# Kernel tuning notes

Hardware: AMD Instinct MI355X
Metric: run time of the kernel (lower is better)

Reference implementation:

```python
import jax, jax.numpy as jnp
import numpy as np
import math

B_SZ, T, D_IN, D_OUT, N = 8, 4096, 128, 128, 256
MAX_PHASE, RMIN, RMAX = math.pi, 0.0, 1.0


def setup_inputs() -> dict:
    key = jax.random.key(0)
    ks = jax.random.split(key, 9)
    x = jax.random.normal(ks[0], (B_SZ, T, D_IN), dtype=jnp.float32)
    # lambda parameterization exactly as in LRU.__init__
    u1 = jax.random.uniform(ks[1], (N,), minval=1e-4, maxval=1.0)
    u2 = jax.random.uniform(ks[2], (N,), minval=1e-4, maxval=1.0)
    nu_log = jnp.log(-0.5 * jnp.log(u1 * (RMAX + RMIN) * (RMAX - RMIN) + RMIN ** 2))
    theta_log = jnp.log(MAX_PHASE * u2)
    lam_abs = jnp.exp(-jnp.exp(nu_log))
    gamma_log = jnp.log(jnp.sqrt(1.0 - jnp.square(lam_abs)))
    B_re = jax.random.normal(ks[3], (N, D_IN)) / math.sqrt(2 * D_IN)
    B_im = jax.random.normal(ks[4], (N, D_IN)) / math.sqrt(2 * D_IN)
    C_re = jax.random.normal(ks[5], (D_OUT, N)) / math.sqrt(N)
    C_im = jax.random.normal(ks[6], (D_OUT, N)) / math.sqrt(N)
    D = jax.random.normal(ks[7], (D_OUT, D_IN)) / math.sqrt(D_IN)
    return {"x": x, "nu_log": nu_log, "theta_log": theta_log, "gamma_log": gamma_log,
            "B_re": B_re, "B_im": B_im, "C_re": C_re, "C_im": C_im, "D": D}


def _binary_op_diag(e1, e2):
    a1, b1 = e1
    a2, b2 = e2
    return a1 * a2, a2 * b1 + b2


def reference(x, nu_log, theta_log, gamma_log, B_re, B_im, C_re, C_im, D):
    # ss_params()
    lam_abs = jnp.exp(-jnp.exp(nu_log))
    phase = jnp.exp(theta_log)
    lam = (lam_abs * jnp.cos(phase) + 1j * (lam_abs * jnp.sin(phase))).astype(jnp.complex64)  # [N]
    gammas = jnp.exp(gamma_log)[:, None]
    Bc = (gammas * (B_re + 1j * B_im)).astype(jnp.complex64)  # [N, D_IN]
    Cc = (C_re + 1j * C_im).astype(jnp.complex64)             # [D_OUT, N]
    # diagonal complex linear recurrence via associative scan over time
    Bu = x.astype(Bc.dtype) @ Bc.T                            # [B, T, N] complex
    lam_el = jnp.broadcast_to(lam, Bu.shape)                  # [B, T, N]
    _, states = jax.lax.associative_scan(_binary_op_diag, (lam_el, Bu), axis=1)
    y = jnp.real(states @ Cc.T) + x @ D.T                     # [B, T, D_OUT]
    return y
```

## Files before the change

### kernel.cpp

```cpp
#include <hip/hip_runtime.h>
#include <math.h>

#define B_SZ 8
#define T_LEN 4096
#define D_IN 128
#define D_OUT 128
#define N_ST 256
#define BT (B_SZ * T_LEN)
#define CHUNK 64
#define NCHUNK (T_LEN / CHUNK)
#define NBLK (B_SZ * NCHUNK)

typedef __attribute__((ext_vector_type(8))) short short8;
typedef __attribute__((ext_vector_type(4))) float f32x4;
typedef unsigned int uint;
typedef unsigned short ushort;

static __device__ __forceinline__ short f2bf(float f) {
  union { float f; uint u; } v; v.f = f;
  uint r = v.u + 0x7FFFu + ((v.u >> 16) & 1u);
  return (short)(r >> 16);
}
static __device__ __forceinline__ float bf2f(uint h) {
  union { uint u; float f; } v; v.u = h << 16;
  return v.f;
}
static __device__ __forceinline__ uint pack2(float a, float b) {
  return (uint)(ushort)f2bf(a) | ((uint)(ushort)f2bf(b) << 16);
}

__global__ __launch_bounds__(256) void k0_setup(
    const float* __restrict__ nu_log, const float* __restrict__ theta_log,
    const float* __restrict__ gamma_log,
    const float* __restrict__ B_re, const float* __restrict__ B_im,
    const float* __restrict__ C_re, const float* __restrict__ C_im,
    const float* __restrict__ Dm,
    short* __restrict__ Wf1, short* __restrict__ Wf2,
    float2* __restrict__ lampow2) {
  int blk = blockIdx.x;
  if (blk < 320) {
    int idx = blk * 256 + threadIdx.x;
    if (idx < 16 * 512 * 8) {
      int j = idx & 7, col = (idx >> 3) & 511, kg = idx >> 12;
      int k = kg * 8 + j;
      int n = col >> 1, ri = col & 1;
      float g = expf(gamma_log[n]);
      float v = g * (ri ? B_im[n * D_IN + k] : B_re[n * D_IN + k]);
      Wf1[idx] = f2bf(v);
    }
    if (idx < 80 * 128 * 8) {
      int j = idx & 7, d = (idx >> 3) & 127, kg = idx >> 10;
      int k = kg * 8 + j;
      float v;
      if (k < 512) {
        int n = k >> 1;
        v = (k & 1) ? -C_im[d * N_ST + n] : C_re[d * N_ST + n];
      } else {
        v = Dm[d * D_IN + (k - 512)];
      }
      Wf2[idx] = f2bf(v);
    }
  } else {
    int j = blk - 320;
    int n = threadIdx.x;
    float e_nu = expf(nu_log[n]);
    float phase = expf(theta_log[n]);
    float r = expf(-(float)j * e_nu);
    float a = (float)j * phase;
    float2 v; v.x = r * cosf(a); v.y = r * sinf(a);
    lampow2[j * N_ST + n] = v;
  }
}

__global__ __launch_bounds__(256, 2) void kA(
    const float* __restrict__ x, const short* __restrict__ Wf1,
    const float2* __restrict__ lampow2,
    uint* __restrict__ states, float2* __restrict__ E) {
  __shared__ short bu[64 * 520];

  int bc = blockIdx.x;
  size_t row0 = (size_t)bc * CHUNK;
  int tid = threadIdx.x;
  int lane = tid & 63, w = tid >> 6;
  int m = lane & 15, q = lane >> 4;

  f32x4 acc[32];
#pragma unroll
  for (int ct = 0; ct < 32; ++ct) acc[ct] = (f32x4){0.f, 0.f, 0.f, 0.f};

  const float* xrow = x + (row0 + 16 * w + m) * D_IN;

  for (int ks = 0; ks < 4; ++ks) {
    float4 xa = *(const float4*)(xrow + 32 * ks + 8 * q);
    float4 xb = *(const float4*)(xrow + 32 * ks + 8 * q + 4);
    short8 af;
    af[0] = f2bf(xa.x); af[1] = f2bf(xa.y); af[2] = f2bf(xa.z); af[3] = f2bf(xa.w);
    af[4] = f2bf(xb.x); af[5] = f2bf(xb.y); af[6] = f2bf(xb.z); af[7] = f2bf(xb.w);
    const short* wbase = Wf1 + ((size_t)(4 * ks + q) * 512 + m) * 8;
#pragma unroll
    for (int ct = 0; ct < 32; ++ct) {
      short8 bf = *(const short8*)(wbase + 16 * ct * 8);
      acc[ct] = __builtin_amdgcn_mfma_f32_16x16x32_bf16(af, bf, acc[ct], 0, 0, 0);
    }
  }

#pragma unroll
  for (int ct = 0; ct < 32; ++ct) {
#pragma unroll
    for (int r = 0; r < 4; ++r) {
      bu[(16 * w + 4 * q + r) * 520 + 16 * ct + m] = f2bf(acc[ct][r]);
    }
  }
  __syncthreads();

  int n = tid;
  float2 lam = lampow2[N_ST + n];
  float sre = 0.f, sim = 0.f;
  uint* sg = states + row0 * N_ST + n;
  for (int j = 0; j < CHUNK; ++j) {
    uint p = ((const uint*)(bu + j * 520))[n];
    float br = bf2f(p & 0xffffu), bi = bf2f(p >> 16);
    float nr = fmaf(lam.x, sre, fmaf(-lam.y, sim, br));
    float ni = fmaf(lam.x, sim, fmaf(lam.y, sre, bi));
    sre = nr; sim = ni;
    sg[(size_t)j * N_ST] = pack2(sre, sim);
  }
  float2 e; e.x = sre; e.y = sim;
  E[bc * N_ST + n] = e;
}

__global__ __launch_bounds__(256) void kB(
    const float2* __restrict__ E, const float2* __restrict__ lampow2,
    float2* __restrict__ P) {
  int g = blockIdx.x * 256 + threadIdx.x;
  int n = g & (N_ST - 1);
  int b = g >> 8;
  float2 lamL = lampow2[CHUNK * N_ST + n];
  float cre = 0.f, cim = 0.f;
  for (int c = 0; c < NCHUNK; ++c) {
    int i = (b * NCHUNK + c) * N_ST + n;
    float2 pv; pv.x = cre; pv.y = cim;
    P[i] = pv;
    float2 e = E[i];
    float nre = fmaf(lamL.x, cre, fmaf(-lamL.y, cim, e.x));
    float nim = fmaf(lamL.x, cim, fmaf(lamL.y, cre, e.y));
    cre = nre; cim = nim;
  }
}

__global__ __launch_bounds__(256, 2) void kC(
    const float* __restrict__ x, const uint* __restrict__ states,
    const float2* __restrict__ P, const float2* __restrict__ lampow2,
    const short* __restrict__ Wf2, float* __restrict__ y) {
  __shared__ short As[64 * 640];

  int bc = blockIdx.x;
  size_t row0 = (size_t)bc * CHUNK;
  int tid = threadIdx.x;

  {
    int n = tid;
    float2 p = P[bc * N_ST + n];
    int g = n >> 2;
    int koff = (2 * n) & 7;
    for (int row = 0; row < CHUNK; ++row) {
      uint sp = states[(row0 + row) * N_ST + n];
      float2 lp = lampow2[(row + 1) * N_ST + n];
      float sr = bf2f(sp & 0xffffu) + lp.x * p.x - lp.y * p.y;
      float si = bf2f(sp >> 16) + lp.x * p.y + lp.y * p.x;
      int gp = (g & ~7) | ((g + row) & 7);
      *(uint*)(As + row * 640 + gp * 8 + koff) = pack2(sr, si);
    }
  }
  {
    int kxp = tid & 63, r0 = tid >> 6;
    int k = 512 + 2 * kxp;
    int g = k >> 3, koff = k & 7;
    for (int rr = 0; rr < 16; ++rr) {
      int row = r0 * 16 + rr;
      float2 xv = *(const float2*)(x + (row0 + row) * D_IN + 2 * kxp);
      int gp = (g & ~7) | ((g + row) & 7);
      *(uint*)(As + row * 640 + gp * 8 + koff) = pack2(xv.x, xv.y);
    }
  }
  __syncthreads();

  int lane = tid & 63, w = tid >> 6;
  int m = lane & 15, q = lane >> 4;
  int arow = 16 * w + m;

  f32x4 acc[8];
#pragma unroll
  for (int ct = 0; ct < 8; ++ct) acc[ct] = (f32x4){0.f, 0.f, 0.f, 0.f};

  for (int ks = 0; ks < 20; ++ks) {
    int g = 4 * ks + q;
    int gp = (g & ~7) | ((g + arow) & 7);
    short8 af = *(const short8*)(As + arow * 640 + gp * 8);
    const short* wbase = Wf2 + ((size_t)g * 128 + m) * 8;
#pragma unroll
    for (int ct = 0; ct < 8; ++ct) {
      short8 bf = *(const short8*)(wbase + 16 * ct * 8);
      acc[ct] = __builtin_amdgcn_mfma_f32_16x16x32_bf16(af, bf, acc[ct], 0, 0, 0);
    }
  }

#pragma unroll
  for (int ct = 0; ct < 8; ++ct) {
#pragma unroll
    for (int r = 0; r < 4; ++r) {
      y[(row0 + 16 * w + 4 * q + r) * D_OUT + 16 * ct + m] = acc[ct][r];
    }
  }
}

extern "C" void kernel_launch(void* const* d_in, const int* in_sizes, int n_in,
                              void* d_out, int out_size, void* d_ws, size_t ws_size,
                              hipStream_t stream) {
  const float* x         = (const float*)d_in[0];
  const float* nu_log    = (const float*)d_in[1];
  const float* theta_log = (const float*)d_in[2];
  const float* gamma_log = (const float*)d_in[3];
  const float* B_re      = (const float*)d_in[4];
  const float* B_im      = (const float*)d_in[5];
  const float* C_re      = (const float*)d_in[6];
  const float* C_im      = (const float*)d_in[7];
  const float* Dm        = (const float*)d_in[8];
  float* y = (float*)d_out;

  char* wp = (char*)d_ws;
  float2* lampow2 = (float2*)wp; wp += (size_t)(CHUNK + 1) * N_ST * sizeof(float2);
  short*  Wf1     = (short*)wp;  wp += (size_t)16 * 512 * 8 * sizeof(short);
  short*  Wf2     = (short*)wp;  wp += (size_t)80 * 128 * 8 * sizeof(short);
  float2* E       = (float2*)wp; wp += (size_t)NBLK * N_ST * sizeof(float2);
  float2* P       = (float2*)wp; wp += (size_t)NBLK * N_ST * sizeof(float2);
  uint*   states  = (uint*)wp;   wp += (size_t)BT * N_ST * sizeof(uint);

  hipLaunchKernelGGL(k0_setup, dim3(385), dim3(256), 0, stream,
                     nu_log, theta_log, gamma_log, B_re, B_im, C_re, C_im, Dm,
                     Wf1, Wf2, lampow2);
  hipLaunchKernelGGL(kA, dim3(NBLK), dim3(256), 0, stream,
                     x, Wf1, lampow2, states, E);
  hipLaunchKernelGGL(kB, dim3(B_SZ * N_ST / 256), dim3(256), 0, stream,
                     E, lampow2, P);
  hipLaunchKernelGGL(kC, dim3(NBLK), dim3(256), 0, stream,
                     x, states, P, lampow2, Wf2, y);
}
```

Measured before the change: 141.4 us.

## Fold inter-chunk carry scan into output kernel, drop separate scan launch

Removes the small kB kernel that serially scanned chunk end-states to produce per-chunk carries. Each kC block now recomputes its own carry by walking all earlier chunk end-states of its batch, which saves one launch and the P buffer round trip. In exchange the work becomes redundant: later chunks do up to 63 dependent complex FMA steps with global loads, which lengthens the tail of kC.

```diff
diff --git a/kernel.cpp b/kernel.cpp
--- a/kernel.cpp
+++ b/kernel.cpp
@@ -129,28 +129,9 @@
   E[bc * N_ST + n] = e;
 }
 
-__global__ __launch_bounds__(256) void kB(
-    const float2* __restrict__ E, const float2* __restrict__ lampow2,
-    float2* __restrict__ P) {
-  int g = blockIdx.x * 256 + threadIdx.x;
-  int n = g & (N_ST - 1);
-  int b = g >> 8;
-  float2 lamL = lampow2[CHUNK * N_ST + n];
-  float cre = 0.f, cim = 0.f;
-  for (int c = 0; c < NCHUNK; ++c) {
-    int i = (b * NCHUNK + c) * N_ST + n;
-    float2 pv; pv.x = cre; pv.y = cim;
-    P[i] = pv;
-    float2 e = E[i];
-    float nre = fmaf(lamL.x, cre, fmaf(-lamL.y, cim, e.x));
-    float nim = fmaf(lamL.x, cim, fmaf(lamL.y, cre, e.y));
-    cre = nre; cim = nim;
-  }
-}
-
 __global__ __launch_bounds__(256, 2) void kC(
     const float* __restrict__ x, const uint* __restrict__ states,
-    const float2* __restrict__ P, const float2* __restrict__ lampow2,
+    const float2* __restrict__ E, const float2* __restrict__ lampow2,
     const short* __restrict__ Wf2, float* __restrict__ y) {
   __shared__ short As[64 * 640];
 
@@ -158,16 +139,27 @@
   size_t row0 = (size_t)bc * CHUNK;
   int tid = threadIdx.x;
 
+  int n = tid;
+  float pre = 0.f, pim = 0.f;
   {
-    int n = tid;
-    float2 p = P[bc * N_ST + n];
+    float2 lamL = lampow2[CHUNK * N_ST + n];
+    int c = bc & (NCHUNK - 1), b = bc >> 6;
+    for (int j = 0; j < c; ++j) {
+      float2 e = E[(size_t)((b << 6) + j) * N_ST + n];
+      float nre = fmaf(lamL.x, pre, fmaf(-lamL.y, pim, e.x));
+      float nim = fmaf(lamL.x, pim, fmaf(lamL.y, pre, e.y));
+      pre = nre; pim = nim;
+    }
+  }
+
+  {
     int g = n >> 2;
     int koff = (2 * n) & 7;
     for (int row = 0; row < CHUNK; ++row) {
       uint sp = states[(row0 + row) * N_ST + n];
       float2 lp = lampow2[(row + 1) * N_ST + n];
-      float sr = bf2f(sp & 0xffffu) + lp.x * p.x - lp.y * p.y;
-      float si = bf2f(sp >> 16) + lp.x * p.y + lp.y * p.x;
+      float sr = bf2f(sp & 0xffffu) + lp.x * pre - lp.y * pim;
+      float si = bf2f(sp >> 16) + lp.x * pim + lp.y * pre;
       int gp = (g & ~7) | ((g + row) & 7);
       *(uint*)(As + row * 640 + gp * 8 + koff) = pack2(sr, si);
     }
@@ -233,7 +225,6 @@
   short*  Wf1     = (short*)wp;  wp += (size_t)16 * 512 * 8 * sizeof(short);
   short*  Wf2     = (short*)wp;  wp += (size_t)80 * 128 * 8 * sizeof(short);
   float2* E       = (float2*)wp; wp += (size_t)NBLK * N_ST * sizeof(float2);
-  float2* P       = (float2*)wp; wp += (size_t)NBLK * N_ST * sizeof(float2);
   uint*   states  = (uint*)wp;   wp += (size_t)BT * N_ST * sizeof(uint);
 
   hipLaunchKernelGGL(k0_setup, dim3(385), dim3(256), 0, stream,
@@ -241,8 +232,6 @@
                      Wf1, Wf2, lampow2);
   hipLaunchKernelGGL(kA, dim3(NBLK), dim3(256), 0, stream,
                      x, Wf1, lampow2, states, E);
-  hipLaunchKernelGGL(kB, dim3(B_SZ * N_ST / 256), dim3(256), 0, stream,
-                     E, lampow2, P);
   hipLaunchKernelGGL(kC, dim3(NBLK), dim3(256), 0, stream,
-                     x, states, P, lampow2, Wf2, y);
-}
+                     x, states, E, lampow2, Wf2, y);
+}
```

Result: slower. 148.0 us (+4.7%).

## Pre-convert x to bf16 once, split kC into half-chunks with vectorized state fixup

Applied to the files above, without the earlier changes.

The setup kernel now also converts x to a bf16 copy, and kA and kC read that copy instead of converting fp32 on the fly. kC is split into two blocks per chunk with 32 rows each, which halves its shared memory and raises the occupancy hint to 4. The state correction loop now handles four states per thread with 128-bit loads and stores. This adds an extra bf16 write and read of x in exchange for less fp32 traffic and better parallelism in kC.

```diff
diff --git a/kernel.cpp b/kernel.cpp
--- a/kernel.cpp
+++ b/kernel.cpp
@@ -30,13 +30,14 @@
 }
 
 __global__ __launch_bounds__(256) void k0_setup(
+    const float* __restrict__ x,
     const float* __restrict__ nu_log, const float* __restrict__ theta_log,
     const float* __restrict__ gamma_log,
     const float* __restrict__ B_re, const float* __restrict__ B_im,
     const float* __restrict__ C_re, const float* __restrict__ C_im,
     const float* __restrict__ Dm,
     short* __restrict__ Wf1, short* __restrict__ Wf2,
-    float2* __restrict__ lampow2) {
+    float2* __restrict__ lampow2, short* __restrict__ xbf) {
   int blk = blockIdx.x;
   if (blk < 320) {
     int idx = blk * 256 + threadIdx.x;
@@ -60,7 +61,7 @@
       }
       Wf2[idx] = f2bf(v);
     }
-  } else {
+  } else if (blk < 385) {
     int j = blk - 320;
     int n = threadIdx.x;
     float e_nu = expf(nu_log[n]);
@@ -69,11 +70,19 @@
     float a = (float)j * phase;
     float2 v; v.x = r * cosf(a); v.y = r * sinf(a);
     lampow2[j * N_ST + n] = v;
+  } else {
+    size_t i = (size_t)(blk - 385) * 256 + threadIdx.x;
+    const float4* x4 = (const float4*)x;
+    float4 a = x4[2 * i], b = x4[2 * i + 1];
+    uint4 u;
+    u.x = pack2(a.x, a.y); u.y = pack2(a.z, a.w);
+    u.z = pack2(b.x, b.y); u.w = pack2(b.z, b.w);
+    ((uint4*)xbf)[i] = u;
   }
 }
 
 __global__ __launch_bounds__(256, 2) void kA(
-    const float* __restrict__ x, const short* __restrict__ Wf1,
+    const short* __restrict__ xbf, const short* __restrict__ Wf1,
     const float2* __restrict__ lampow2,
     uint* __restrict__ states, float2* __restrict__ E) {
   __shared__ short bu[64 * 520];
@@ -88,14 +97,10 @@
 #pragma unroll
   for (int ct = 0; ct < 32; ++ct) acc[ct] = (f32x4){0.f, 0.f, 0.f, 0.f};
 
-  const float* xrow = x + (row0 + 16 * w + m) * D_IN;
+  const short* xrow = xbf + (row0 + 16 * w + m) * D_IN;
 
   for (int ks = 0; ks < 4; ++ks) {
-    float4 xa = *(const float4*)(xrow + 32 * ks + 8 * q);
-    float4 xb = *(const float4*)(xrow + 32 * ks + 8 * q + 4);
-    short8 af;
-    af[0] = f2bf(xa.x); af[1] = f2bf(xa.y); af[2] = f2bf(xa.z); af[3] = f2bf(xa.w);
-    af[4] = f2bf(xb.x); af[5] = f2bf(xb.y); af[6] = f2bf(xb.z); af[7] = f2bf(xb.w);
+    short8 af = *(const short8*)(xrow + 32 * ks + 8 * q);
     const short* wbase = Wf1 + ((size_t)(4 * ks + q) * 512 + m) * 8;
 #pragma unroll
     for (int ct = 0; ct < 32; ++ct) {
@@ -148,50 +153,78 @@
   }
 }
 
-__global__ __launch_bounds__(256, 2) void kC(
-    const float* __restrict__ x, const uint* __restrict__ states,
+__global__ __launch_bounds__(256, 4) void kC(
+    const short* __restrict__ xbf, const uint* __restrict__ states,
     const float2* __restrict__ P, const float2* __restrict__ lampow2,
     const short* __restrict__ Wf2, float* __restrict__ y) {
-  __shared__ short As[64 * 640];
-
-  int bc = blockIdx.x;
-  size_t row0 = (size_t)bc * CHUNK;
+  __shared__ short As[32 * 640];
+
+  int blk = blockIdx.x;
+  int bc = blk >> 1;
+  int j0 = (blk & 1) * 32;
+  size_t row0 = (size_t)blk * 32;
   int tid = threadIdx.x;
-
-  {
-    int n = tid;
-    float2 p = P[bc * N_ST + n];
-    int g = n >> 2;
-    int koff = (2 * n) & 7;
-    for (int row = 0; row < CHUNK; ++row) {
-      uint sp = states[(row0 + row) * N_ST + n];
-      float2 lp = lampow2[(row + 1) * N_ST + n];
-      float sr = bf2f(sp & 0xffffu) + lp.x * p.x - lp.y * p.y;
-      float si = bf2f(sp >> 16) + lp.x * p.y + lp.y * p.x;
-      int gp = (g & ~7) | ((g + row) & 7);
-      *(uint*)(As + row * 640 + gp * 8 + koff) = pack2(sr, si);
-    }
-  }
+  int n4 = tid & 63, rblk = tid >> 6;
+
+  float4 pA = *(const float4*)(P + (size_t)bc * N_ST + 4 * n4);
+  float4 pB = *(const float4*)(P + (size_t)bc * N_ST + 4 * n4 + 2);
+
   {
     int kxp = tid & 63, r0 = tid >> 6;
     int k = 512 + 2 * kxp;
     int g = k >> 3, koff = k & 7;
-    for (int rr = 0; rr < 16; ++rr) {
-      int row = r0 * 16 + rr;
-      float2 xv = *(const float2*)(x + (row0 + row) * D_IN + 2 * kxp);
+    for (int rr = 0; rr < 8; ++rr) {
+      int row = r0 * 8 + rr;
+      uint xv = *(const uint*)(xbf + (row0 + row) * D_IN + 2 * kxp);
       int gp = (g & ~7) | ((g + row) & 7);
-      *(uint*)(As + row * 640 + gp * 8 + koff) = pack2(xv.x, xv.y);
+      *(uint*)(As + row * 640 + gp * 8 + koff) = xv;
+    }
+  }
+
+  {
+#pragma unroll
+    for (int rr = 0; rr < 8; ++rr) {
+      int row = rblk * 8 + rr;
+      int j = j0 + row;
+      uint4 sp = *(const uint4*)(states + ((row0 + row) * N_ST + 4 * n4));
+      float4 lpa = *(const float4*)(lampow2 + ((size_t)(j + 1) * N_ST + 4 * n4));
+      float4 lpb = *(const float4*)(lampow2 + ((size_t)(j + 1) * N_ST + 4 * n4 + 2));
+      uint4 outv;
+      {
+        float sr = bf2f(sp.x & 0xffffu) + lpa.x * pA.x - lpa.y * pA.y;
+        float si = bf2f(sp.x >> 16)     + lpa.x * pA.y + lpa.y * pA.x;
+        outv.x = pack2(sr, si);
+      }
+      {
+        float sr = bf2f(sp.y & 0xffffu) + lpa.z * pA.z - lpa.w * pA.w;
+        float si = bf2f(sp.y >> 16)     + lpa.z * pA.w + lpa.w * pA.z;
+        outv.y = pack2(sr, si);
+      }
+      {
+        float sr = bf2f(sp.z & 0xffffu) + lpb.x * pB.x - lpb.y * pB.y;
+        float si = bf2f(sp.z >> 16)     + lpb.x * pB.y + lpb.y * pB.x;
+        outv.z = pack2(sr, si);
+      }
+      {
+        float sr = bf2f(sp.w & 0xffffu) + lpb.z * pB.z - lpb.w * pB.w;
+        float si = bf2f(sp.w >> 16)     + lpb.z * pB.w + lpb.w * pB.z;
+        outv.w = pack2(sr, si);
+      }
+      int g = n4;
+      int gp = (g & ~7) | ((g + row) & 7);
+      *(uint4*)(As + row * 640 + gp * 8) = outv;
     }
   }
   __syncthreads();
 
   int lane = tid & 63, w = tid >> 6;
   int m = lane & 15, q = lane >> 4;
-  int arow = 16 * w + m;
-
-  f32x4 acc[8];
-#pragma unroll
-  for (int ct = 0; ct < 8; ++ct) acc[ct] = (f32x4){0.f, 0.f, 0.f, 0.f};
+  int rw = w & 1, ch = w >> 1;
+  int arow = 16 * rw + m;
+
+  f32x4 acc[4];
+#pragma unroll
+  for (int ct = 0; ct < 4; ++ct) acc[ct] = (f32x4){0.f, 0.f, 0.f, 0.f};
 
   for (int ks = 0; ks < 20; ++ks) {
     int g = 4 * ks + q;
@@ -199,17 +232,19 @@
     short8 af = *(const short8*)(As + arow * 640 + gp * 8);
     const short* wbase = Wf2 + ((size_t)g * 128 + m) * 8;
 #pragma unroll
-    for (int ct = 0; ct < 8; ++ct) {
-      short8 bf = *(const short8*)(wbase + 16 * ct * 8);
+    for (int ct = 0; ct < 4; ++ct) {
+      int ctg = 4 * ch + ct;
+      short8 bf = *(const short8*)(wbase + 16 * ctg * 8);
       acc[ct] = __builtin_amdgcn_mfma_f32_16x16x32_bf16(af, bf, acc[ct], 0, 0, 0);
     }
   }
 
 #pragma unroll
-  for (int ct = 0; ct < 8; ++ct) {
+  for (int ct = 0; ct < 4; ++ct) {
+    int ctg = 4 * ch + ct;
 #pragma unroll
     for (int r = 0; r < 4; ++r) {
-      y[(row0 + 16 * w + 4 * q + r) * D_OUT + 16 * ct + m] = acc[ct][r];
+      y[(row0 + 16 * rw + 4 * q + r) * D_OUT + 16 * ctg + m] = acc[ct][r];
     }
   }
 }
@@ -234,15 +269,16 @@
   short*  Wf2     = (short*)wp;  wp += (size_t)80 * 128 * 8 * sizeof(short);
   float2* E       = (float2*)wp; wp += (size_t)NBLK * N_ST * sizeof(float2);
   float2* P       = (float2*)wp; wp += (size_t)NBLK * N_ST * sizeof(float2);
+  short*  xbf     = (short*)wp;  wp += (size_t)BT * D_IN * sizeof(short);
   uint*   states  = (uint*)wp;   wp += (size_t)BT * N_ST * sizeof(uint);
 
-  hipLaunchKernelGGL(k0_setup, dim3(385), dim3(256), 0, stream,
-                     nu_log, theta_log, gamma_log, B_re, B_im, C_re, C_im, Dm,
-                     Wf1, Wf2, lampow2);
+  hipLaunchKernelGGL(k0_setup, dim3(385 + BT * D_IN / 8 / 256), dim3(256), 0, stream,
+                     x, nu_log, theta_log, gamma_log, B_re, B_im, C_re, C_im,
+                     Dm, Wf1, Wf2, lampow2, xbf);
   hipLaunchKernelGGL(kA, dim3(NBLK), dim3(256), 0, stream,
-                     x, Wf1, lampow2, states, E);
+                     xbf, Wf1, lampow2, states, E);
   hipLaunchKernelGGL(kB, dim3(B_SZ * N_ST / 256), dim3(256), 0, stream,
                      E, lampow2, P);
-  hipLaunchKernelGGL(kC, dim3(NBLK), dim3(256), 0, stream,
-                     x, states, P, lampow2, Wf2, y);
-}
+  hipLaunchKernelGGL(kC, dim3(2 * NBLK), dim3(256), 0, stream,
+                     xbf, states, P, lampow2, Wf2, y);
+}
```

Measured after the change: 134.4 us, median of 2. 5.0% less time.
